# Kernel optimization log

Hardware: AMD Instinct MI355X
Metric: run time of the kernel (lower is better)

The kernel has to match this reference:

```python
import jax, jax.numpy as jnp
import numpy as np

B, L, H, NH = 32, 512, 256, 4
DH = H // NH
EPS = 1e-12


def setup_inputs() -> dict:
    key = jax.random.key(0)
    ks = jax.random.split(key, 24)
    p = lambda k, shape: 0.02 * jax.random.normal(k, shape, dtype=jnp.float32)
    return {
        "input_tensor": jax.random.normal(ks[0], (B, L, H), dtype=jnp.float32),
        # sorted positive timestamps (seconds-like scale)
        "time_seq": jnp.sort(jax.random.uniform(ks[1], (B, L), dtype=jnp.float32) * 100.0, axis=-1),
        "attention_mask": jnp.zeros((B, 1, L, L), dtype=jnp.float32),
        "item_seq_len": jnp.clip(jax.random.randint(ks[2], (B,), 0, L), 2, L),
        "Wq": p(ks[3], (H, H)), "bq": jnp.zeros((H,), jnp.float32),
        "Wk": p(ks[4], (H, H)), "bk": jnp.zeros((H,), jnp.float32),
        "Wv": p(ks[5], (H, H)), "bv": jnp.zeros((H,), jnp.float32),
        "Wd": p(ks[6], (H, H)), "bd": jnp.zeros((H,), jnp.float32),
        "ln_g": jnp.ones((H,), jnp.float32), "ln_b": jnp.zeros((H,), jnp.float32),
        "Wtq": p(ks[7], (H, H)), "btq": jnp.zeros((H,), jnp.float32),
        "tw1": p(ks[8], (L, L)), "tb1": p(ks[9], (L, L)),
        "tow1": p(ks[10], (L, L)), "tow2": p(ks[11], (L, L)), "tob": p(ks[12], (L, L)),
        "Wt": p(ks[13], (1, 2 * H)), "bt": jnp.zeros((1,), jnp.float32),
    }


def reference(input_tensor, time_seq, attention_mask, item_seq_len,
              Wq, bq, Wk, bk, Wv, bv, Wd, bd, ln_g, ln_b,
              Wtq, btq, tw1, tb1, tow1, tow2, tob, Wt, bt):
    x = input_tensor  # (B, L, H)

    def heads(t):  # (B,L,H) -> (B,NH,L,DH)
        return t.reshape(B, L, NH, DH).transpose(0, 2, 1, 3)

    q = heads(x @ Wq.T + bq)
    k = heads(x @ Wk.T + bk)
    v = heads(x @ Wv.T + bv)

    scores = jnp.einsum('bhqd,bhkd->bhqk', q, k)  # (B,NH,L,L)

    # --- time decay gate ---
    tq = x @ Wtq.T + btq                                  # (B,L,H)
    time_query_key = jnp.tanh(jnp.einsum('bqh,bkh->bqk', tq, x))  # (B,L,L)
    diff = jnp.abs(time_seq[:, :, None] - time_seq[:, None, :])   # |t_i - t_j|
    decay = jnp.tanh(jnp.log1p(diff) * tw1 + tb1)
    decay_gate = tow1 * decay + tow2 * time_query_key + tob       # (B,L,L)
    time_attn = jax.nn.sigmoid(decay_gate)[:, None, :, :]         # (B,1,L,L)

    scores = scores * time_attn / jnp.sqrt(jnp.float32(DH)) + attention_mask
    probs = jax.nn.softmax(scores, axis=-1)

    ctx = jnp.einsum('bhqk,bhkd->bhqd', probs, v)
    ctx = ctx.transpose(0, 2, 1, 3).reshape(B, L, H)

    hs = ctx @ Wd.T + bd + x
    mu = jnp.mean(hs, axis=-1, keepdims=True)
    var = jnp.var(hs, axis=-1, keepdims=True)
    hs = (hs - mu) / jnp.sqrt(var + EPS) * ln_g + ln_b   # (B,L,H)

    bidx = jnp.arange(B)
    emb1 = hs[bidx, item_seq_len - 1]  # (B,H)
    emb2 = hs[bidx, item_seq_len - 2]  # (B,H)
    pred_intervals = jnp.concatenate([emb1, emb2], axis=1) @ Wt.T + bt  # (B,1)
    return hs, pred_intervals
```

## Files before the change

kernel.cpp:

```cpp
#include <hip/hip_runtime.h>
#include <math.h>

#define Bn 32
#define Ln 512
#define Hn 256
#define NHn 4
#define DHn 64

typedef __attribute__((ext_vector_type(8))) short bf16x8;
typedef __attribute__((ext_vector_type(4))) float f32x4;
typedef unsigned int uint32;

__device__ __forceinline__ short f2b(float f) {
    union { float f; uint32 u; } v; v.f = f;
    uint32 r = (v.u + 0x7FFFu + ((v.u >> 16) & 1u)) >> 16;
    return (short)r;
}
__device__ __forceinline__ float b2f(short h) {
    union { uint32 u; float f; } v; v.u = ((uint32)(unsigned short)h) << 16;
    return v.f;
}
__device__ __forceinline__ float fast_tanh(float x) {
    float e = __expf(2.f * x);
    return 1.f - 2.f * __builtin_amdgcn_rcpf(e + 1.f);
}
__device__ __forceinline__ float fast_sigmoid(float x) {
    return __builtin_amdgcn_rcpf(1.f + __expf(-x));
}

__global__ __launch_bounds__(256) void conv_kernel(
    const float* __restrict__ x,
    const float* __restrict__ Wq, const float* __restrict__ Wk,
    const float* __restrict__ Wv, const float* __restrict__ Wtq,
    const float* __restrict__ Wd,
    short* __restrict__ xb, short* __restrict__ wb)
{
    const size_t NLH = (size_t)Bn * Ln * Hn;
    size_t i4 = ((size_t)blockIdx.x * 256 + threadIdx.x) * 4;
    if (i4 < NLH) {
        float4 v = *(const float4*)(x + i4);
        short4 o; o.x = f2b(v.x); o.y = f2b(v.y); o.z = f2b(v.z); o.w = f2b(v.w);
        *(short4*)(xb + i4) = o;
    } else {
        size_t off = i4 - NLH;
        int w = (int)(off >> 16);
        size_t wi = off & 65535;
        const float* src = (w == 0) ? Wq : (w == 1) ? Wk : (w == 2) ? Wv : (w == 3) ? Wtq : Wd;
        float4 v = *(const float4*)(src + wi);
        short4 o; o.x = f2b(v.x); o.y = f2b(v.y); o.z = f2b(v.z); o.w = f2b(v.w);
        *(short4*)(wb + off) = o;
    }
}

struct Acc { f32x4 t[4]; };

__device__ __forceinline__ void gemm_tile_64(
    const short* __restrict__ A,
    const short* __restrict__ Bm,
    int K, short* As, short* Bs, Acc& acc)
{
    const int tid = threadIdx.x;
    const int lane = tid & 63, w = tid >> 6;
    const int quad = lane >> 4, lm = lane & 15;
    const int srow = tid >> 3;
    const int slot = tid & 7;

    for (int k0 = 0; k0 < K; k0 += 64) {
        __syncthreads();
#pragma unroll
        for (int iss = 0; iss < 2; ++iss) {
            int r = srow + iss * 32;
            bf16x8 av = *(const bf16x8*)(A + (size_t)r * K + k0 + slot * 8);
            bf16x8 bv = *(const bf16x8*)(Bm + (size_t)r * K + k0 + slot * 8);
            *(bf16x8*)(As + r * 72 + slot * 8) = av;
            *(bf16x8*)(Bs + r * 72 + slot * 8) = bv;
        }
        __syncthreads();
#pragma unroll
        for (int ks = 0; ks < 2; ++ks) {
            bf16x8 a = *(const bf16x8*)(As + (w * 16 + lm) * 72 + ks * 32 + quad * 8);
#pragma unroll
            for (int kt = 0; kt < 4; ++kt) {
                bf16x8 b = *(const bf16x8*)(Bs + (kt * 16 + lm) * 72 + ks * 32 + quad * 8);
                acc.t[kt] = __builtin_amdgcn_mfma_f32_16x16x32_bf16(a, b, acc.t[kt], 0, 0, 0);
            }
        }
    }
}

__global__ __launch_bounds__(256) void proj_kernel(
    const short* __restrict__ xb, const short* __restrict__ wb,
    const float* __restrict__ bq, const float* __restrict__ bk,
    const float* __restrict__ bv, const float* __restrict__ btq,
    short* __restrict__ qb, short* __restrict__ kb,
    short* __restrict__ vt, short* __restrict__ tqb)
{
    __shared__ short As[64 * 72];
    __shared__ short Bs[64 * 72];
    const int tensor = blockIdx.x >> 2;
    const int ncol0 = (blockIdx.x & 3) * 64;
    const int m0 = blockIdx.y * 64;
    const short* A = xb + (size_t)m0 * Hn;
    const short* Bw = wb + (size_t)tensor * 65536 + (size_t)ncol0 * Hn;
    const float* bias = (tensor == 0) ? bq : (tensor == 1) ? bk : (tensor == 2) ? bv : btq;

    Acc acc;
#pragma unroll
    for (int i = 0; i < 4; ++i) acc.t[i] = (f32x4){0.f, 0.f, 0.f, 0.f};
    gemm_tile_64(A, Bw, Hn, As, Bs, acc);

    const int lane = threadIdx.x & 63, w = threadIdx.x >> 6;
    const int quad = lane >> 4, lm = lane & 15;

    if (tensor == 2) {
#pragma unroll
        for (int kt = 0; kt < 4; ++kt) {
            int n = ncol0 + kt * 16 + lm;
            float bs = bv[n];
            int h = n >> 6, d = n & 63;
#pragma unroll
            for (int r = 0; r < 4; ++r) {
                int row = m0 + w * 16 + quad * 4 + r;
                int bb = row >> 9, l = row & 511;
                vt[((size_t)(bb * NHn + h) * DHn + d) * Ln + l] = f2b(acc.t[kt][r] + bs);
            }
        }
    } else {
        short* out = (tensor == 0) ? qb : (tensor == 1) ? kb : tqb;
#pragma unroll
        for (int kt = 0; kt < 4; ++kt) {
            int n = ncol0 + kt * 16 + lm;
            float bs = bias[n];
#pragma unroll
            for (int r = 0; r < 4; ++r) {
                int row = m0 + w * 16 + quad * 4 + r;
                out[(size_t)row * Hn + n] = f2b(acc.t[kt][r] + bs);
            }
        }
    }
}

__global__ __launch_bounds__(256) void gate_kernel(
    const short* __restrict__ tqb, const short* __restrict__ xb,
    const float* __restrict__ tseq,
    const float* __restrict__ tw1, const float* __restrict__ tb1,
    const float* __restrict__ tow1, const float* __restrict__ tow2,
    const float* __restrict__ tob, const float* __restrict__ mask,
    uint32* __restrict__ gateb)
{
    __shared__ short As[64 * 72];
    __shared__ short Bs[64 * 72];
    const int b = blockIdx.z;
    const int m0 = blockIdx.y * 64, n0 = blockIdx.x * 64;
    const short* A = tqb + ((size_t)b * Ln + m0) * Hn;
    const short* Bw = xb + ((size_t)b * Ln + n0) * Hn;

    Acc acc;
#pragma unroll
    for (int i = 0; i < 4; ++i) acc.t[i] = (f32x4){0.f, 0.f, 0.f, 0.f};
    gemm_tile_64(A, Bw, Hn, As, Bs, acc);

    const int lane = threadIdx.x & 63, w = threadIdx.x >> 6;
    const int quad = lane >> 4, lm = lane & 15;
    const float* ts = tseq + (size_t)b * Ln;
    const float* mk = mask + (size_t)b * Ln * Ln;
    uint32* go = gateb + (size_t)b * Ln * Ln;
    float ti[4];
#pragma unroll
    for (int r = 0; r < 4; ++r) ti[r] = ts[m0 + w * 16 + quad * 4 + r];
#pragma unroll
    for (int kt = 0; kt < 4; ++kt) {
        int j = n0 + kt * 16 + lm;
        float tj = ts[j];
#pragma unroll
        for (int r = 0; r < 4; ++r) {
            int i = m0 + w * 16 + quad * 4 + r;
            size_t ij = (size_t)i * Ln + j;
            float lg = __logf(1.f + fabsf(ti[r] - tj));
            float dec = fast_tanh(lg * tw1[ij] + tb1[ij]);
            float tqk = fast_tanh(acc.t[kt][r]);
            float dg = tow1[ij] * dec + tow2[ij] * tqk + tob[ij];
            float g = 0.125f * fast_sigmoid(dg);
            uint32 pk = ((uint32)(unsigned short)f2b(mk[ij]) << 16)
                      |  (uint32)(unsigned short)f2b(g);
            go[ij] = pk;
        }
    }
}

__global__ __launch_bounds__(256) void flash_mfma(
    const short* __restrict__ qb, const short* __restrict__ kb,
    const short* __restrict__ vt, const uint32* __restrict__ gateb,
    short* __restrict__ ctxb)
{
    __shared__ short Ks[64 * 72];
    __shared__ short Vt[64 * 72];
    __shared__ short Ps[4 * 16 * 72];
    const int q0 = blockIdx.x * 64;
    const int h = blockIdx.y, b = blockIdx.z;
    const int tid = threadIdx.x;
    const int w = tid >> 6, lane = tid & 63;
    const int quad = lane >> 4, lm = lane & 15;

    bf16x8 qf0, qf1;
    {
        const short* qrow = qb + ((size_t)(b * Ln + q0 + w * 16 + lm)) * Hn + h * DHn;
        qf0 = *(const bf16x8*)(qrow + quad * 8);
        qf1 = *(const bf16x8*)(qrow + 32 + quad * 8);
    }

    f32x4 o[4];
#pragma unroll
    for (int i = 0; i < 4; ++i) o[i] = (f32x4){0.f, 0.f, 0.f, 0.f};
    float m_run[4] = {-INFINITY, -INFINITY, -INFINITY, -INFINITY};
    float l_run[4] = {0.f, 0.f, 0.f, 0.f};
    const uint32* gm_base = gateb + (size_t)b * Ln * Ln;
    const int qrow0 = q0 + w * 16 + quad * 4;
    const short* vbase = vt + (size_t)(b * NHn + h) * DHn * Ln;

    for (int k0 = 0; k0 < Ln; k0 += 64) {
        __syncthreads();
        {
            int srow = tid >> 3, slot = tid & 7;
#pragma unroll
            for (int iss = 0; iss < 2; ++iss) {
                int r = srow + iss * 32;
                bf16x8 kv = *(const bf16x8*)(kb + ((size_t)(b * Ln + k0 + r)) * Hn + h * DHn + slot * 8);
                *(bf16x8*)(Ks + r * 72 + slot * 8) = kv;
                bf16x8 vv = *(const bf16x8*)(vbase + (size_t)r * Ln + k0 + slot * 8);
                *(bf16x8*)(Vt + r * 72 + slot * 8) = vv;
            }
        }
        __syncthreads();

        f32x4 s[4];
#pragma unroll
        for (int kt = 0; kt < 4; ++kt) {
            s[kt] = (f32x4){0.f, 0.f, 0.f, 0.f};
            bf16x8 b0 = *(const bf16x8*)(Ks + (kt * 16 + lm) * 72 + quad * 8);
            s[kt] = __builtin_amdgcn_mfma_f32_16x16x32_bf16(qf0, b0, s[kt], 0, 0, 0);
            bf16x8 b1 = *(const bf16x8*)(Ks + (kt * 16 + lm) * 72 + 32 + quad * 8);
            s[kt] = __builtin_amdgcn_mfma_f32_16x16x32_bf16(qf1, b1, s[kt], 0, 0, 0);
        }

        float mnew[4];
#pragma unroll
        for (int r = 0; r < 4; ++r) mnew[r] = m_run[r];
#pragma unroll
        for (int kt = 0; kt < 4; ++kt) {
            int col = k0 + kt * 16 + lm;
#pragma unroll
            for (int r = 0; r < 4; ++r) {
                uint32 gm = gm_base[(size_t)(qrow0 + r) * Ln + col];
                float g  = b2f((short)(gm & 0xFFFFu));
                float mv = b2f((short)(gm >> 16));
                float sv = s[kt][r] * g + mv;
                s[kt][r] = sv;
                mnew[r] = fmaxf(mnew[r], sv);
            }
        }
        float alpha[4], rsum[4];
#pragma unroll
        for (int r = 0; r < 4; ++r) {
#pragma unroll
            for (int off = 1; off < 16; off <<= 1)
                mnew[r] = fmaxf(mnew[r], __shfl_xor(mnew[r], off, 64));
            alpha[r] = __expf(m_run[r] - mnew[r]);
            m_run[r] = mnew[r];
            rsum[r] = 0.f;
        }
        float p[4][4];
#pragma unroll
        for (int kt = 0; kt < 4; ++kt)
#pragma unroll
            for (int r = 0; r < 4; ++r) {
                float pv = __expf(s[kt][r] - m_run[r]);
                p[kt][r] = pv;
                rsum[r] += pv;
            }
#pragma unroll
        for (int r = 0; r < 4; ++r) {
#pragma unroll
            for (int off = 1; off < 16; off <<= 1) rsum[r] += __shfl_xor(rsum[r], off, 64);
            l_run[r] = l_run[r] * alpha[r] + rsum[r];
#pragma unroll
            for (int ot = 0; ot < 4; ++ot) o[ot][r] *= alpha[r];
        }
        short* pw = Ps + w * 16 * 72;
#pragma unroll
        for (int kt = 0; kt < 4; ++kt)
#pragma unroll
            for (int r = 0; r < 4; ++r)
                pw[(quad * 4 + r) * 72 + kt * 16 + lm] = f2b(p[kt][r]);

#pragma unroll
        for (int ks = 0; ks < 2; ++ks) {
            bf16x8 pa = *(const bf16x8*)(pw + lm * 72 + ks * 32 + quad * 8);
#pragma unroll
            for (int ot = 0; ot < 4; ++ot) {
                bf16x8 vv = *(const bf16x8*)(Vt + (ot * 16 + lm) * 72 + ks * 32 + quad * 8);
                o[ot] = __builtin_amdgcn_mfma_f32_16x16x32_bf16(pa, vv, o[ot], 0, 0, 0);
            }
        }
    }

    float inv[4];
#pragma unroll
    for (int r = 0; r < 4; ++r) inv[r] = 1.0f / l_run[r];
#pragma unroll
    for (int ot = 0; ot < 4; ++ot) {
        int d = h * DHn + ot * 16 + lm;
#pragma unroll
        for (int r = 0; r < 4; ++r) {
            int row = b * Ln + qrow0 + r;
            ctxb[(size_t)row * Hn + d] = f2b(o[ot][r] * inv[r]);
        }
    }
}

__global__ __launch_bounds__(256) void outproj_kernel(
    const short* __restrict__ ctxb, const short* __restrict__ wdb,
    const float* __restrict__ bd, const float* __restrict__ x,
    float* __restrict__ out)
{
    __shared__ short As[64 * 72];
    __shared__ short Bs[64 * 72];
    const int n0 = blockIdx.x * 64, m0 = blockIdx.y * 64;
    Acc acc;
#pragma unroll
    for (int i = 0; i < 4; ++i) acc.t[i] = (f32x4){0.f, 0.f, 0.f, 0.f};
    gemm_tile_64(ctxb + (size_t)m0 * Hn, wdb + (size_t)n0 * Hn, Hn, As, Bs, acc);

    const int lane = threadIdx.x & 63, w = threadIdx.x >> 6;
    const int quad = lane >> 4, lm = lane & 15;
#pragma unroll
    for (int kt = 0; kt < 4; ++kt) {
        int n = n0 + kt * 16 + lm;
        float bs = bd[n];
#pragma unroll
        for (int r = 0; r < 4; ++r) {
            int row = m0 + w * 16 + quad * 4 + r;
            out[(size_t)row * Hn + n] = acc.t[kt][r] + bs + x[(size_t)row * Hn + n];
        }
    }
}

__global__ __launch_bounds__(256) void ln_kernel(float* __restrict__ hs,
                                                 const float* __restrict__ g,
                                                 const float* __restrict__ bta)
{
    const int row = blockIdx.x, t = threadIdx.x;
    float v = hs[(size_t)row * Hn + t];
    float s1 = v, s2 = v * v;
#pragma unroll
    for (int off = 32; off > 0; off >>= 1) {
        s1 += __shfl_xor(s1, off, 64);
        s2 += __shfl_xor(s2, off, 64);
    }
    __shared__ float red[8];
    if ((t & 63) == 0) { red[t >> 6] = s1; red[4 + (t >> 6)] = s2; }
    __syncthreads();
    float sum = red[0] + red[1] + red[2] + red[3];
    float sq  = red[4] + red[5] + red[6] + red[7];
    float mu  = sum * (1.f / 256.f);
    float var = sq * (1.f / 256.f) - mu * mu;
    float rstd = rsqrtf(var + 1e-12f);
    hs[(size_t)row * Hn + t] = (v - mu) * rstd * g[t] + bta[t];
}

__global__ __launch_bounds__(256) void pred_kernel(const float* __restrict__ hs,
                                                   const int* __restrict__ lens,
                                                   const float* __restrict__ Wt,
                                                   const float* __restrict__ bt,
                                                   float* __restrict__ pred)
{
    const int b = blockIdx.x, t = threadIdx.x;
    int len = lens[b];
    float e1 = hs[((size_t)b * Ln + (len - 1)) * Hn + t];
    float e2 = hs[((size_t)b * Ln + (len - 2)) * Hn + t];
    float v = e1 * Wt[t] + e2 * Wt[Hn + t];
#pragma unroll
    for (int off = 32; off > 0; off >>= 1) v += __shfl_xor(v, off, 64);
    __shared__ float ps[4];
    if ((t & 63) == 0) ps[t >> 6] = v;
    __syncthreads();
    if (t == 0) pred[b] = ps[0] + ps[1] + ps[2] + ps[3] + bt[0];
}

extern "C" void kernel_launch(void* const* d_in, const int* in_sizes, int n_in,
                              void* d_out, int out_size, void* d_ws, size_t ws_size,
                              hipStream_t stream) {
    (void)in_sizes; (void)n_in; (void)out_size; (void)ws_size;
    const float* x    = (const float*)d_in[0];
    const float* tseq = (const float*)d_in[1];
    const float* mask = (const float*)d_in[2];
    const int*   lens = (const int*)d_in[3];
    const float* Wq = (const float*)d_in[4];  const float* bq = (const float*)d_in[5];
    const float* Wk = (const float*)d_in[6];  const float* bk = (const float*)d_in[7];
    const float* Wv = (const float*)d_in[8];  const float* bv = (const float*)d_in[9];
    const float* Wd = (const float*)d_in[10]; const float* bd = (const float*)d_in[11];
    const float* ln_g = (const float*)d_in[12]; const float* ln_b = (const float*)d_in[13];
    const float* Wtq = (const float*)d_in[14]; const float* btq = (const float*)d_in[15];
    const float* tw1 = (const float*)d_in[16]; const float* tb1 = (const float*)d_in[17];
    const float* tow1 = (const float*)d_in[18]; const float* tow2 = (const float*)d_in[19];
    const float* tob = (const float*)d_in[20];
    const float* Wt = (const float*)d_in[21]; const float* bt = (const float*)d_in[22];

    const size_t NLH = (size_t)Bn * Ln * Hn;
    short* ws = (short*)d_ws;
    short* xb    = ws;
    short* wb    = xb + NLH;
    short* qb    = wb + 5 * 65536;
    short* kb    = qb + NLH;
    short* vt    = kb + NLH;
    short* tqb   = vt + NLH;
    uint32* gateb = (uint32*)(tqb + NLH);
    short* ctxb  = tqb;
    float* out   = (float*)d_out;

    dim3 blk(256);
    conv_kernel<<<dim3(4416), blk, 0, stream>>>(x, Wq, Wk, Wv, Wtq, Wd, xb, wb);
    proj_kernel<<<dim3(16, 256), blk, 0, stream>>>(xb, wb, bq, bk, bv, btq, qb, kb, vt, tqb);
    gate_kernel<<<dim3(8, 8, Bn), blk, 0, stream>>>(tqb, xb, tseq, tw1, tb1, tow1, tow2, tob, mask, gateb);
    flash_mfma<<<dim3(8, NHn, Bn), blk, 0, stream>>>(qb, kb, vt, gateb, ctxb);
    outproj_kernel<<<dim3(4, 256), blk, 0, stream>>>(ctxb, wb + 4 * 65536, bd, x, out);
    ln_kernel<<<dim3(Bn * Ln), blk, 0, stream>>>(out, ln_g, ln_b);
    pred_kernel<<<dim3(Bn), blk, 0, stream>>>(out, lens, Wt, bt, out + NLH);
}
```

Before: 246.2 us.

## Prefetch GEMM tiles in registers, split gate/mask, fuse outproj with LayerNorm

Adds register-level prefetch of the next K/V or A/B tiles in the shared GEMM helper and the flash attention loop, so global loads overlap with MFMA work. The gate kernel now writes only a bf16 gate, and the flash kernel reads the fp32 mask directly instead of a packed gate+mask word. The output projection and LayerNorm are fused into one kernel where each block computes full 256-column rows, removing a separate LN pass over the output. The trade-offs are more mask bytes read per head in flash and fewer, heavier blocks in the fused outproj.

Result: slower. 272.1 us (+10.5%).

```diff
diff --git a/kernel.cpp b/kernel.cpp
--- a/kernel.cpp
+++ b/kernel.cpp
@@ -54,10 +54,11 @@
 
 struct Acc { f32x4 t[4]; };
 
+template<int K>
 __device__ __forceinline__ void gemm_tile_64(
     const short* __restrict__ A,
     const short* __restrict__ Bm,
-    int K, short* As, short* Bs, Acc& acc)
+    short* As, short* Bs, Acc& acc)
 {
     const int tid = threadIdx.x;
     const int lane = tid & 63, w = tid >> 6;
@@ -65,17 +66,31 @@
     const int srow = tid >> 3;
     const int slot = tid & 7;
 
+    bf16x8 av[2], bv[2];
+#pragma unroll
+    for (int iss = 0; iss < 2; ++iss) {
+        int r = srow + iss * 32;
+        av[iss] = *(const bf16x8*)(A + (size_t)r * K + slot * 8);
+        bv[iss] = *(const bf16x8*)(Bm + (size_t)r * K + slot * 8);
+    }
+#pragma unroll
     for (int k0 = 0; k0 < K; k0 += 64) {
         __syncthreads();
 #pragma unroll
         for (int iss = 0; iss < 2; ++iss) {
             int r = srow + iss * 32;
-            bf16x8 av = *(const bf16x8*)(A + (size_t)r * K + k0 + slot * 8);
-            bf16x8 bv = *(const bf16x8*)(Bm + (size_t)r * K + k0 + slot * 8);
-            *(bf16x8*)(As + r * 72 + slot * 8) = av;
-            *(bf16x8*)(Bs + r * 72 + slot * 8) = bv;
+            *(bf16x8*)(As + r * 72 + slot * 8) = av[iss];
+            *(bf16x8*)(Bs + r * 72 + slot * 8) = bv[iss];
         }
         __syncthreads();
+        if (k0 + 64 < K) {
+#pragma unroll
+            for (int iss = 0; iss < 2; ++iss) {
+                int r = srow + iss * 32;
+                av[iss] = *(const bf16x8*)(A + (size_t)r * K + k0 + 64 + slot * 8);
+                bv[iss] = *(const bf16x8*)(Bm + (size_t)r * K + k0 + 64 + slot * 8);
+            }
+        }
 #pragma unroll
         for (int ks = 0; ks < 2; ++ks) {
             bf16x8 a = *(const bf16x8*)(As + (w * 16 + lm) * 72 + ks * 32 + quad * 8);
@@ -107,7 +122,7 @@
     Acc acc;
 #pragma unroll
     for (int i = 0; i < 4; ++i) acc.t[i] = (f32x4){0.f, 0.f, 0.f, 0.f};
-    gemm_tile_64(A, Bw, Hn, As, Bs, acc);
+    gemm_tile_64<Hn>(A, Bw, As, Bs, acc);
 
     const int lane = threadIdx.x & 63, w = threadIdx.x >> 6;
     const int quad = lane >> 4, lm = lane & 15;
@@ -145,8 +160,8 @@
     const float* __restrict__ tseq,
     const float* __restrict__ tw1, const float* __restrict__ tb1,
     const float* __restrict__ tow1, const float* __restrict__ tow2,
-    const float* __restrict__ tob, const float* __restrict__ mask,
-    uint32* __restrict__ gateb)
+    const float* __restrict__ tob,
+    short* __restrict__ gateb)
 {
     __shared__ short As[64 * 72];
     __shared__ short Bs[64 * 72];
@@ -158,13 +173,12 @@
     Acc acc;
 #pragma unroll
     for (int i = 0; i < 4; ++i) acc.t[i] = (f32x4){0.f, 0.f, 0.f, 0.f};
-    gemm_tile_64(A, Bw, Hn, As, Bs, acc);
+    gemm_tile_64<Hn>(A, Bw, As, Bs, acc);
 
     const int lane = threadIdx.x & 63, w = threadIdx.x >> 6;
     const int quad = lane >> 4, lm = lane & 15;
     const float* ts = tseq + (size_t)b * Ln;
-    const float* mk = mask + (size_t)b * Ln * Ln;
-    uint32* go = gateb + (size_t)b * Ln * Ln;
+    short* go = gateb + (size_t)b * Ln * Ln;
     float ti[4];
 #pragma unroll
     for (int r = 0; r < 4; ++r) ti[r] = ts[m0 + w * 16 + quad * 4 + r];
@@ -181,17 +195,15 @@
             float tqk = fast_tanh(acc.t[kt][r]);
             float dg = tow1[ij] * dec + tow2[ij] * tqk + tob[ij];
             float g = 0.125f * fast_sigmoid(dg);
-            uint32 pk = ((uint32)(unsigned short)f2b(mk[ij]) << 16)
-                      |  (uint32)(unsigned short)f2b(g);
-            go[ij] = pk;
+            go[ij] = f2b(g);
         }
     }
 }
 
 __global__ __launch_bounds__(256) void flash_mfma(
     const short* __restrict__ qb, const short* __restrict__ kb,
-    const short* __restrict__ vt, const uint32* __restrict__ gateb,
-    short* __restrict__ ctxb)
+    const short* __restrict__ vt, const short* __restrict__ gateb,
+    const float* __restrict__ mask, short* __restrict__ ctxb)
 {
     __shared__ short Ks[64 * 72];
     __shared__ short Vt[64 * 72];
@@ -201,6 +213,7 @@
     const int tid = threadIdx.x;
     const int w = tid >> 6, lane = tid & 63;
     const int quad = lane >> 4, lm = lane & 15;
+    const int srow = tid >> 3, slot = tid & 7;
 
     bf16x8 qf0, qf1;
     {
@@ -214,24 +227,37 @@
     for (int i = 0; i < 4; ++i) o[i] = (f32x4){0.f, 0.f, 0.f, 0.f};
     float m_run[4] = {-INFINITY, -INFINITY, -INFINITY, -INFINITY};
     float l_run[4] = {0.f, 0.f, 0.f, 0.f};
-    const uint32* gm_base = gateb + (size_t)b * Ln * Ln;
+    const short* gr_base = gateb + (size_t)b * Ln * Ln;
+    const float* mk_base = mask + (size_t)b * Ln * Ln;
     const int qrow0 = q0 + w * 16 + quad * 4;
+    const short* kbase = kb + ((size_t)(b * Ln)) * Hn + h * DHn;
     const short* vbase = vt + (size_t)(b * NHn + h) * DHn * Ln;
+
+    bf16x8 kr[2], vr[2];
+#pragma unroll
+    for (int iss = 0; iss < 2; ++iss) {
+        int r = srow + iss * 32;
+        kr[iss] = *(const bf16x8*)(kbase + (size_t)r * Hn + slot * 8);
+        vr[iss] = *(const bf16x8*)(vbase + (size_t)r * Ln + slot * 8);
+    }
 
     for (int k0 = 0; k0 < Ln; k0 += 64) {
         __syncthreads();
-        {
-            int srow = tid >> 3, slot = tid & 7;
+#pragma unroll
+        for (int iss = 0; iss < 2; ++iss) {
+            int r = srow + iss * 32;
+            *(bf16x8*)(Ks + r * 72 + slot * 8) = kr[iss];
+            *(bf16x8*)(Vt + r * 72 + slot * 8) = vr[iss];
+        }
+        __syncthreads();
+        if (k0 + 64 < Ln) {
 #pragma unroll
             for (int iss = 0; iss < 2; ++iss) {
                 int r = srow + iss * 32;
-                bf16x8 kv = *(const bf16x8*)(kb + ((size_t)(b * Ln + k0 + r)) * Hn + h * DHn + slot * 8);
-                *(bf16x8*)(Ks + r * 72 + slot * 8) = kv;
-                bf16x8 vv = *(const bf16x8*)(vbase + (size_t)r * Ln + k0 + slot * 8);
-                *(bf16x8*)(Vt + r * 72 + slot * 8) = vv;
-            }
-        }
-        __syncthreads();
+                kr[iss] = *(const bf16x8*)(kbase + (size_t)(k0 + 64 + r) * Hn + slot * 8);
+                vr[iss] = *(const bf16x8*)(vbase + (size_t)r * Ln + k0 + 64 + slot * 8);
+            }
+        }
 
         f32x4 s[4];
 #pragma unroll
@@ -251,9 +277,8 @@
             int col = k0 + kt * 16 + lm;
 #pragma unroll
             for (int r = 0; r < 4; ++r) {
-                uint32 gm = gm_base[(size_t)(qrow0 + r) * Ln + col];
-                float g  = b2f((short)(gm & 0xFFFFu));
-                float mv = b2f((short)(gm >> 16));
+                float g  = b2f(gr_base[(size_t)(qrow0 + r) * Ln + col]);
+                float mv = mk_base[(size_t)(qrow0 + r) * Ln + col];
                 float sv = s[kt][r] * g + mv;
                 s[kt][r] = sv;
                 mnew[r] = fmaxf(mnew[r], sv);
@@ -318,54 +343,113 @@
     }
 }
 
-__global__ __launch_bounds__(256) void outproj_kernel(
+__global__ __launch_bounds__(256) void outproj_ln_kernel(
     const short* __restrict__ ctxb, const short* __restrict__ wdb,
     const float* __restrict__ bd, const float* __restrict__ x,
+    const float* __restrict__ g, const float* __restrict__ beta,
     float* __restrict__ out)
 {
-    __shared__ short As[64 * 72];
+    __shared__ short As[64 * 264];
     __shared__ short Bs[64 * 72];
-    const int n0 = blockIdx.x * 64, m0 = blockIdx.y * 64;
-    Acc acc;
-#pragma unroll
-    for (int i = 0; i < 4; ++i) acc.t[i] = (f32x4){0.f, 0.f, 0.f, 0.f};
-    gemm_tile_64(ctxb + (size_t)m0 * Hn, wdb + (size_t)n0 * Hn, Hn, As, Bs, acc);
-
-    const int lane = threadIdx.x & 63, w = threadIdx.x >> 6;
+    const int m0 = blockIdx.x * 64;
+    const int tid = threadIdx.x;
+    const int lane = tid & 63, w = tid >> 6;
     const int quad = lane >> 4, lm = lane & 15;
-#pragma unroll
-    for (int kt = 0; kt < 4; ++kt) {
-        int n = n0 + kt * 16 + lm;
-        float bs = bd[n];
-#pragma unroll
-        for (int r = 0; r < 4; ++r) {
-            int row = m0 + w * 16 + quad * 4 + r;
-            out[(size_t)row * Hn + n] = acc.t[kt][r] + bs + x[(size_t)row * Hn + n];
-        }
-    }
-}
-
-__global__ __launch_bounds__(256) void ln_kernel(float* __restrict__ hs,
-                                                 const float* __restrict__ g,
-                                                 const float* __restrict__ bta)
-{
-    const int row = blockIdx.x, t = threadIdx.x;
-    float v = hs[(size_t)row * Hn + t];
-    float s1 = v, s2 = v * v;
-#pragma unroll
-    for (int off = 32; off > 0; off >>= 1) {
-        s1 += __shfl_xor(s1, off, 64);
-        s2 += __shfl_xor(s2, off, 64);
-    }
-    __shared__ float red[8];
-    if ((t & 63) == 0) { red[t >> 6] = s1; red[4 + (t >> 6)] = s2; }
-    __syncthreads();
-    float sum = red[0] + red[1] + red[2] + red[3];
-    float sq  = red[4] + red[5] + red[6] + red[7];
-    float mu  = sum * (1.f / 256.f);
-    float var = sq * (1.f / 256.f) - mu * mu;
-    float rstd = rsqrtf(var + 1e-12f);
-    hs[(size_t)row * Hn + t] = (v - mu) * rstd * g[t] + bta[t];
+    const int srow = tid >> 3, slot = tid & 7;
+
+#pragma unroll
+    for (int iss = 0; iss < 2; ++iss) {
+        int r = srow + iss * 32;
+#pragma unroll
+        for (int c = 0; c < 4; ++c) {
+            bf16x8 av = *(const bf16x8*)(ctxb + (size_t)(m0 + r) * Hn + c * 64 + slot * 8);
+            *(bf16x8*)(As + r * 264 + c * 64 + slot * 8) = av;
+        }
+    }
+
+    f32x4 acc[4][4];
+#pragma unroll
+    for (int i = 0; i < 4; ++i)
+#pragma unroll
+        for (int j = 0; j < 4; ++j) acc[i][j] = (f32x4){0.f, 0.f, 0.f, 0.f};
+
+    bf16x8 bv[2];
+#pragma unroll
+    for (int iss = 0; iss < 2; ++iss)
+        bv[iss] = *(const bf16x8*)(wdb + (size_t)(srow + iss * 32) * Hn + slot * 8);
+
+#pragma unroll
+    for (int nt = 0; nt < 4; ++nt) {
+#pragma unroll
+        for (int k0 = 0; k0 < Hn; k0 += 64) {
+#pragma unroll
+            for (int iss = 0; iss < 2; ++iss)
+                *(bf16x8*)(Bs + (srow + iss * 32) * 72 + slot * 8) = bv[iss];
+            __syncthreads();
+            int k1 = (k0 + 64 < Hn) ? k0 + 64 : 0;
+            int nt1 = (k0 + 64 < Hn) ? nt : nt + 1;
+            if (nt1 < 4) {
+                const short* wsrc = wdb + (size_t)(nt1 * 64) * Hn + k1;
+#pragma unroll
+                for (int iss = 0; iss < 2; ++iss)
+                    bv[iss] = *(const bf16x8*)(wsrc + (size_t)(srow + iss * 32) * Hn + slot * 8);
+            }
+#pragma unroll
+            for (int ks = 0; ks < 2; ++ks) {
+                bf16x8 a = *(const bf16x8*)(As + (w * 16 + lm) * 264 + k0 + ks * 32 + quad * 8);
+#pragma unroll
+                for (int kt = 0; kt < 4; ++kt) {
+                    bf16x8 bb = *(const bf16x8*)(Bs + (kt * 16 + lm) * 72 + ks * 32 + quad * 8);
+                    acc[nt][kt] = __builtin_amdgcn_mfma_f32_16x16x32_bf16(a, bb, acc[nt][kt], 0, 0, 0);
+                }
+            }
+            __syncthreads();
+        }
+    }
+
+    const int rl0 = w * 16 + quad * 4;
+    float s1[4] = {0.f, 0.f, 0.f, 0.f}, s2[4] = {0.f, 0.f, 0.f, 0.f};
+#pragma unroll
+    for (int nt = 0; nt < 4; ++nt)
+#pragma unroll
+        for (int kt = 0; kt < 4; ++kt) {
+            int col = nt * 64 + kt * 16 + lm;
+            float bdv = bd[col];
+#pragma unroll
+            for (int r = 0; r < 4; ++r) {
+                float xv = x[(size_t)(m0 + rl0 + r) * Hn + col];
+                float hv = acc[nt][kt][r] + bdv + xv;
+                acc[nt][kt][r] = hv;
+                s1[r] += hv;
+                s2[r] += hv * hv;
+            }
+        }
+#pragma unroll
+    for (int r = 0; r < 4; ++r) {
+#pragma unroll
+        for (int off = 1; off < 16; off <<= 1) {
+            s1[r] += __shfl_xor(s1[r], off, 64);
+            s2[r] += __shfl_xor(s2[r], off, 64);
+        }
+    }
+    float mu[4], rstd[4];
+#pragma unroll
+    for (int r = 0; r < 4; ++r) {
+        mu[r] = s1[r] * (1.f / 256.f);
+        float var = s2[r] * (1.f / 256.f) - mu[r] * mu[r];
+        rstd[r] = rsqrtf(var + 1e-12f);
+    }
+#pragma unroll
+    for (int nt = 0; nt < 4; ++nt)
+#pragma unroll
+        for (int kt = 0; kt < 4; ++kt) {
+            int col = nt * 64 + kt * 16 + lm;
+            float gv = g[col], bb = beta[col];
+#pragma unroll
+            for (int r = 0; r < 4; ++r)
+                out[(size_t)(m0 + rl0 + r) * Hn + col] =
+                    (acc[nt][kt][r] - mu[r]) * rstd[r] * gv + bb;
+        }
 }
 
 __global__ __launch_bounds__(256) void pred_kernel(const float* __restrict__ hs,
@@ -414,16 +498,15 @@
     short* kb    = qb + NLH;
     short* vt    = kb + NLH;
     short* tqb   = vt + NLH;
-    uint32* gateb = (uint32*)(tqb + NLH);
+    short* gateb = tqb + NLH;
     short* ctxb  = tqb;
     float* out   = (float*)d_out;
 
     dim3 blk(256);
     conv_kernel<<<dim3(4416), blk, 0, stream>>>(x, Wq, Wk, Wv, Wtq, Wd, xb, wb);
     proj_kernel<<<dim3(16, 256), blk, 0, stream>>>(xb, wb, bq, bk, bv, btq, qb, kb, vt, tqb);
-    gate_kernel<<<dim3(8, 8, Bn), blk, 0, stream>>>(tqb, xb, tseq, tw1, tb1, tow1, tow2, tob, mask, gateb);
-    flash_mfma<<<dim3(8, NHn, Bn), blk, 0, stream>>>(qb, kb, vt, gateb, ctxb);
-    outproj_kernel<<<dim3(4, 256), blk, 0, stream>>>(ctxb, wb + 4 * 65536, bd, x, out);
-    ln_kernel<<<dim3(Bn * Ln), blk, 0, stream>>>(out, ln_g, ln_b);
+    gate_kernel<<<dim3(8, 8, Bn), blk, 0, stream>>>(tqb, xb, tseq, tw1, tb1, tow1, tow2, tob, gateb);
+    flash_mfma<<<dim3(8, NHn, Bn), blk, 0, stream>>>(qb, kb, vt, gateb, mask, ctxb);
+    outproj_ln_kernel<<<dim3(256), blk, 0, stream>>>(ctxb, wb + 4 * 65536, bd, x, ln_g, ln_b, out);
     pred_kernel<<<dim3(Bn), blk, 0, stream>>>(out, lens, Wt, bt, out + NLH);
 }
```
